# Kernel tuning notes

Measured on AMD Instinct MI355X. Metric: run time of the kernel, lower is better.

The kernel has to match this reference:

```python
import jax, jax.numpy as jnp
import numpy as np

EPS = 1e-6
K = 20  # n_knn from init


def _vnt_weight(W):
    # VNT linear: rows normalized to sum to 1 (which_norm_VNT='norm') for translation equivariance
    return W / jnp.sum(W, axis=1, keepdims=True)


def _lin(W, x):
    # apply [out,in] weight over channel axis 1 of x: [B, C_in, 3, ...] -> [B, C_out, 3, ...]
    return jnp.einsum('oi,bi...->bo...', W, x)


def _vn_lrelu(x, Wf, Wd, vnt=False):
    # VN(T)LinearLeakyReLU with negative_slope=0.0, no batchnorm. Vector axis is axis 2.
    Wp = _vnt_weight(Wf) if vnt else Wf
    p = _lin(Wp, x)
    d = _lin(Wd, x)
    dot = jnp.sum(p * d, axis=2, keepdims=True)
    dsq = jnp.sum(d * d, axis=2, keepdims=True)
    return jnp.where(dot >= 0, p, p - (dot / (dsq + EPS)) * d)


def _knn(pts, k):
    # pts: [B,N,3] -> indices of k nearest (self included), via -||xi-xj||^2 top_k
    sq = jnp.sum(pts * pts, axis=-1)                      # [B,N]
    inner = jnp.einsum('bnd,bmd->bnm', pts, pts)          # [B,N,N]
    neg_dist = 2.0 * inner - sq[:, :, None] - sq[:, None, :]
    return jax.lax.top_k(neg_dist, k)[1]                  # [B,N,k]


def _graph_feature_cross(x, k):
    # x: [B,3,N] -> edge features [B, 3(feat: nbr-ctr, ctr, cross), 3(vec), N, k]
    pts = jnp.transpose(x, (0, 2, 1))                     # [B,N,3]
    idx = _knn(pts, k)                                    # [B,N,k]
    nbr = jax.vmap(lambda p, i: p[i])(pts, idx)           # [B,N,k,3]
    ctr = jnp.broadcast_to(pts[:, :, None, :], nbr.shape)
    cross = jnp.cross(nbr, ctr)
    feat = jnp.stack([nbr - ctr, ctr, cross], axis=3)     # [B,N,k,3feat,3vec]
    return jnp.transpose(feat, (0, 3, 4, 1, 2))           # [B,3feat,3vec,N,k]


def _forward(x, Wpos_f, Wpos_d, Wc1_f, Wc1_d, Wc2_f, Wc2_d, Wt_f, Wt_d, W1_f, W1_d, W2_f, W2_d, W3):
    feat = _graph_feature_cross(x, K)                     # [B,3,3,N,K]
    h = _vn_lrelu(feat, Wpos_f, Wpos_d, vnt=True)         # [B,64,3,N,K]
    h = h.mean(axis=-1)                                   # mean pool over k -> [B,64,3,N]
    x2 = _vn_lrelu(h, Wc1_f, Wc1_d, vnt=True)             # conv_center_
    xc = _vn_lrelu(x2, Wc2_f, Wc2_d, vnt=True)            # conv_center
    tx = _vn_lrelu(xc, Wt_f, Wt_d, vnt=True)              # conv_trans [B,12,3,N]
    trans_latent = tx.mean(axis=-1)                       # [B,12,3]
    h = h - xc                                            # center features
    h = _vn_lrelu(h, W1_f, W1_d)                          # conv1
    h = _vn_lrelu(h, W2_f, W2_d)                          # conv2
    h = _lin(W3, h)                                       # conv3 (plain VNLinear) [B,116,3,N]
    rot_latent = h.mean(axis=-1)                          # [B,116,3]
    return jnp.concatenate([rot_latent, trans_latent], axis=1)  # [B,128,3]


def setup_inputs() -> dict:
    key = jax.random.key(0)
    ks = jax.random.split(key, 16)
    B, N, C = 4, 4096, 64
    ROT = 116  # c_dim - trans_c_dim

    def w(k, o, i):
        return jax.random.normal(k, (o, i), jnp.float32) * 0.1

    def wt(k, o, i):
        # VNT weights: row sums kept near 1 so normalization is well-conditioned
        return jax.random.normal(k, (o, i), jnp.float32) * 0.02 + 1.0 / i

    return {
        'x': jax.random.normal(ks[0], (B, 3, N), jnp.float32),
        'Wpos_f': wt(ks[1], C, 3), 'Wpos_d': w(ks[2], C, 3),
        'Wc1_f': wt(ks[3], C, C), 'Wc1_d': w(ks[4], C, C),
        'Wc2_f': wt(ks[5], C, C), 'Wc2_d': w(ks[6], C, C),
        'Wt_f': wt(ks[7], 12, C), 'Wt_d': w(ks[8], 12, C),
        'W1_f': w(ks[9], C, C), 'W1_d': w(ks[10], C, C),
        'W2_f': w(ks[11], C, C), 'W2_d': w(ks[12], C, C),
        'W3': w(ks[13], ROT, C),
    }


def reference(x, Wpos_f, Wpos_d, Wc1_f, Wc1_d, Wc2_f, Wc2_d, Wt_f, Wt_d, W1_f, W1_d, W2_f, W2_d, W3):
    return _forward(x, Wpos_f, Wpos_d, Wc1_f, Wc1_d, Wc2_f, Wc2_d, Wt_f, Wt_d, W1_f, W1_d, W2_f, W2_d, W3)
```

## Files before the change

### kernel.cpp

```cpp
#include <hip/hip_runtime.h>

#define NPTS 4096
#define BATCH 4
#define KNN 20
#define ROT 116

__device__ __forceinline__ void vn_lrelu3(float p[3], const float d[3]) {
  float dot = p[0]*d[0] + p[1]*d[1] + p[2]*d[2];
  if (dot < 0.0f) {
    float dsq = d[0]*d[0] + d[1]*d[1] + d[2]*d[2];
    float r = dot / (dsq + 1e-6f);
    p[0] -= r*d[0]; p[1] -= r*d[1]; p[2] -= r*d[2];
  }
}

__global__ __launch_bounds__(256) void knn_edge2_kernel(const float* __restrict__ x,
                                                        const float* __restrict__ Wf,
                                                        const float* __restrict__ Wd,
                                                        float* __restrict__ h) {
  const int blk = blockIdx.x;
  const int rowA = blk << 1, rowB = rowA + 1;
  const int b = rowA >> 12;
  const int iA = rowA & (NPTS - 1), iB = rowB & (NPTS - 1);
  const float* __restrict__ xb = x + b * 3 * NPTS;
  const float cxA = xb[iA], cyA = xb[NPTS + iA], czA = xb[2 * NPTS + iA];
  const float cxB = xb[iB], cyB = xb[NPTS + iB], czB = xb[2 * NPTS + iB];
  const int t = threadIdx.x;
  const int j0 = t << 4;

  __shared__ unsigned int hist[2048];
  __shared__ unsigned int ldA_[384], ldB_[384];
  __shared__ int ljA_[384], ljB_[384];
  __shared__ unsigned int lcount;
  __shared__ int s_BA, s_BB;
  __shared__ unsigned int wtot[4];
  __shared__ int s_nbrA[KNN], s_nbrB[KNN];
  __shared__ float eA[KNN][3][3], eB[KNN][3][3];
  __shared__ float partA[2][64][3], partB[2][64][3];

  for (int k = t; k < 2048; k += 256) hist[k] = 0u;
  if (t == 0) lcount = 0u;
  __syncthreads();

  unsigned int dbA[16], dbB[16];
#pragma unroll
  for (int q = 0; q < 4; ++q) {
    const float4 px = *(const float4*)(xb + j0 + 4 * q);
    const float4 py = *(const float4*)(xb + NPTS + j0 + 4 * q);
    const float4 pz = *(const float4*)(xb + 2 * NPTS + j0 + 4 * q);
    float dx, dy, dz, dd;
    dx = px.x - cxA; dy = py.x - cyA; dz = pz.x - czA;
    dd = dx*dx + dy*dy + dz*dz; dbA[4*q+0] = __float_as_uint(dd);
    dx = px.y - cxA; dy = py.y - cyA; dz = pz.y - czA;
    dd = dx*dx + dy*dy + dz*dz; dbA[4*q+1] = __float_as_uint(dd);
    dx = px.z - cxA; dy = py.z - cyA; dz = pz.z - czA;
    dd = dx*dx + dy*dy + dz*dz; dbA[4*q+2] = __float_as_uint(dd);
    dx = px.w - cxA; dy = py.w - cyA; dz = pz.w - czA;
    dd = dx*dx + dy*dy + dz*dz; dbA[4*q+3] = __float_as_uint(dd);
    dx = px.x - cxB; dy = py.x - cyB; dz = pz.x - czB;
    dd = dx*dx + dy*dy + dz*dz; dbB[4*q+0] = __float_as_uint(dd);
    dx = px.y - cxB; dy = py.y - cyB; dz = pz.y - czB;
    dd = dx*dx + dy*dy + dz*dz; dbB[4*q+1] = __float_as_uint(dd);
    dx = px.z - cxB; dy = py.z - cyB; dz = pz.z - czB;
    dd = dx*dx + dy*dy + dz*dz; dbB[4*q+2] = __float_as_uint(dd);
    dx = px.w - cxB; dy = py.w - cyB; dz = pz.w - czB;
    dd = dx*dx + dy*dy + dz*dz; dbB[4*q+3] = __float_as_uint(dd);
  }
#pragma unroll
  for (int s = 0; s < 16; ++s) {
    atomicAdd(&hist[dbA[s] >> 20], 1u);
    atomicAdd(&hist[dbB[s] >> 20], 0x10000u);
  }
  __syncthreads();

  unsigned int v = 0;
#pragma unroll
  for (int s = 0; s < 8; ++s) v += hist[t * 8 + s];
  const unsigned int myps = v;
  const int lane = t & 63;
#pragma unroll
  for (int off = 1; off < 64; off <<= 1) {
    unsigned int n = (unsigned int)__shfl_up((int)v, off);
    if (lane >= off) v += n;
  }
  if (lane == 63) wtot[t >> 6] = v;
  __syncthreads();
  unsigned int woff = 0;
#pragma unroll
  for (int w = 0; w < 4; ++w) if (w < (t >> 6)) woff += wtot[w];
  const unsigned int cum_in = v + woff;
  const unsigned int cum_ex = cum_in - myps;
  {
    const int ci = (int)(cum_in & 0xffffu), ce = (int)(cum_ex & 0xffffu);
    if (ce < KNN && ci >= KNN) {
      int cum = ce, B = t * 8;
      for (int s = 0; s < 8; ++s) {
        const int hh = (int)(hist[t * 8 + s] & 0xffffu);
        if (cum + hh >= KNN) { B = t * 8 + s; break; }
        cum += hh;
      }
      s_BA = B;
    }
  }
  {
    const int ci = (int)(cum_in >> 16), ce = (int)(cum_ex >> 16);
    if (ce < KNN && ci >= KNN) {
      int cum = ce, B = t * 8;
      for (int s = 0; s < 8; ++s) {
        const int hh = (int)(hist[t * 8 + s] >> 16);
        if (cum + hh >= KNN) { B = t * 8 + s; break; }
        cum += hh;
      }
      s_BB = B;
    }
  }
  __syncthreads();
  const unsigned int BA = (unsigned int)s_BA, BB = (unsigned int)s_BB;
#pragma unroll
  for (int s = 0; s < 16; ++s) {
    if ((dbA[s] >> 20) <= BA) {
      unsigned int old = atomicAdd(&lcount, 1u);
      unsigned int pos = old & 0xffffu;
      if (pos < 384u) { ldA_[pos] = dbA[s]; ljA_[pos] = j0 + s; }
    }
    if ((dbB[s] >> 20) <= BB) {
      unsigned int old = atomicAdd(&lcount, 0x10000u);
      unsigned int pos = old >> 16;
      if (pos < 384u) { ldB_[pos] = dbB[s]; ljB_[pos] = j0 + s; }
    }
  }
  __syncthreads();
  const int nA = min((int)(lcount & 0xffffu), 384);
  const int nB = min((int)(lcount >> 16), 384);
  if (t < 128) {
    for (int idx = t; idx < nA; idx += 128) {
      const unsigned int kd = ldA_[idx]; const int kj = ljA_[idx];
      int rank = 0;
      for (int m = 0; m < nA; ++m) {
        const unsigned int md = ldA_[m];
        rank += (md < kd || (md == kd && ljA_[m] < kj)) ? 1 : 0;
      }
      if (rank < KNN) s_nbrA[rank] = kj;
    }
  } else {
    for (int idx = t - 128; idx < nB; idx += 128) {
      const unsigned int kd = ldB_[idx]; const int kj = ljB_[idx];
      int rank = 0;
      for (int m = 0; m < nB; ++m) {
        const unsigned int md = ldB_[m];
        rank += (md < kd || (md == kd && ljB_[m] < kj)) ? 1 : 0;
      }
      if (rank < KNN) s_nbrB[rank] = kj;
    }
  }
  __syncthreads();

  if (t < KNN) {
    const int j = s_nbrA[t];
    const float nx = xb[j], ny = xb[NPTS + j], nz = xb[2 * NPTS + j];
    eA[t][0][0] = nx - cxA; eA[t][0][1] = ny - cyA; eA[t][0][2] = nz - czA;
    eA[t][1][0] = cxA;      eA[t][1][1] = cyA;      eA[t][1][2] = czA;
    eA[t][2][0] = ny * czA - nz * cyA;
    eA[t][2][1] = nz * cxA - nx * czA;
    eA[t][2][2] = nx * cyA - ny * cxA;
  } else if (t >= 64 && t < 64 + KNN) {
    const int k = t - 64;
    const int j = s_nbrB[k];
    const float nx = xb[j], ny = xb[NPTS + j], nz = xb[2 * NPTS + j];
    eB[k][0][0] = nx - cxB; eB[k][0][1] = ny - cyB; eB[k][0][2] = nz - czB;
    eB[k][1][0] = cxB;      eB[k][1][1] = cyB;      eB[k][1][2] = czB;
    eB[k][2][0] = ny * czB - nz * cyB;
    eB[k][2][1] = nz * cxB - nx * czB;
    eB[k][2][2] = nx * cyB - ny * cxB;
  }
  __syncthreads();

  const int c = t & 63;
  const int half = t >> 7;
  const int kg = (t >> 6) & 1;
  float f0 = Wf[c * 3 + 0], f1 = Wf[c * 3 + 1], f2 = Wf[c * 3 + 2];
  const float s = 1.0f / (f0 + f1 + f2);
  f0 *= s; f1 *= s; f2 *= s;
  const float d0 = Wd[c * 3 + 0], d1 = Wd[c * 3 + 1], d2 = Wd[c * 3 + 2];
  float a0 = 0.f, a1 = 0.f, a2 = 0.f;
  const float (*e)[3][3] = (half == 0) ? eA : eB;
#pragma unroll
  for (int kk = 0; kk < 10; ++kk) {
    const int k = kg * 10 + kk;
    float pv[3], dv[3];
#pragma unroll
    for (int vv = 0; vv < 3; ++vv) {
      pv[vv] = f0 * e[k][0][vv] + f1 * e[k][1][vv] + f2 * e[k][2][vv];
      dv[vv] = d0 * e[k][0][vv] + d1 * e[k][1][vv] + d2 * e[k][2][vv];
    }
    vn_lrelu3(pv, dv);
    a0 += pv[0]; a1 += pv[1]; a2 += pv[2];
  }
  if (half == 0) { partA[kg][c][0] = a0; partA[kg][c][1] = a1; partA[kg][c][2] = a2; }
  else           { partB[kg][c][0] = a0; partB[kg][c][1] = a1; partB[kg][c][2] = a2; }
  __syncthreads();
  if (t < 64) {
    const float inv = 1.0f / KNN;
    float* hp = h + (size_t)rowA * 192 + t * 3;
#pragma unroll
    for (int vv = 0; vv < 3; ++vv)
      hp[vv] = (partA[0][t][vv] + partA[1][t][vv]) * inv;
  } else if (t < 128) {
    const int cc = t - 64;
    const float inv = 1.0f / KNN;
    float* hp = h + (size_t)rowB * 192 + cc * 3;
#pragma unroll
    for (int vv = 0; vv < 3; ++vv)
      hp[vv] = (partB[0][cc][vv] + partB[1][cc][vv]) * inv;
  }
}

template<bool VNT, int MODE>
__global__ __launch_bounds__(256) void layer_batch(
    const float* in, float* out, float* aux,
    const float* __restrict__ Wf, const float* __restrict__ Wd) {
  __shared__ float wfT[64][65], wdT[64][65];
  __shared__ float act[4][4][64][4];
  const int t = threadIdx.x, q = t >> 6, c = t & 63;
  for (int e = t; e < 4096; e += 256) {
    wfT[e & 63][e >> 6] = Wf[e];
    wdT[e & 63][e >> 6] = Wd[e];
  }
  __syncthreads();
  if (VNT) {
    if (t < 64) {
      float s = 0.f;
      for (int i = 0; i < 64; ++i) s += wfT[i][t];
      s = 1.0f / s;
      for (int i = 0; i < 64; ++i) wfT[i][t] *= s;
    }
    __syncthreads();
  }
  const int pbase = (blockIdx.x * 4 + q) * 8;
  float r0 = 0.f, r1 = 0.f, r2 = 0.f;
  for (int pass = 0; pass < 2; ++pass) {
    const int p0 = pbase + pass * 4;
#pragma unroll
    for (int p = 0; p < 4; ++p) {
      const float* ip = in + (size_t)(p0 + p) * 192 + c * 3;
      *(float4*)act[q][p][c] = make_float4(ip[0], ip[1], ip[2], 0.f);
    }
    __builtin_amdgcn_wave_barrier();
    float af[12], ad[12];
#pragma unroll
    for (int e = 0; e < 12; ++e) { af[e] = 0.f; ad[e] = 0.f; }
    for (int i = 0; i < 64; ++i) {
      const float wfv = wfT[i][c];
      const float wdv = wdT[i][c];
#pragma unroll
      for (int p = 0; p < 4; ++p) {
        const float4 hv = *(const float4*)act[q][p][i];
        af[p*3+0] += wfv * hv.x; af[p*3+1] += wfv * hv.y; af[p*3+2] += wfv * hv.z;
        ad[p*3+0] += wdv * hv.x; ad[p*3+1] += wdv * hv.y; ad[p*3+2] += wdv * hv.z;
      }
    }
    __builtin_amdgcn_wave_barrier();
#pragma unroll
    for (int p = 0; p < 4; ++p) {
      float pf[3] = { af[p*3+0], af[p*3+1], af[p*3+2] };
      float pd[3] = { ad[p*3+0], ad[p*3+1], ad[p*3+2] };
      vn_lrelu3(pf, pd);
      const size_t ofs = (size_t)(p0 + p) * 192 + c * 3;
      if (MODE == 0) {
        out[ofs+0] = pf[0]; out[ofs+1] = pf[1]; out[ofs+2] = pf[2];
      } else if (MODE == 1) {
        const float h0 = aux[ofs+0], h1 = aux[ofs+1], h2 = aux[ofs+2];
        aux[ofs+0] = h0 - pf[0]; aux[ofs+1] = h1 - pf[1]; aux[ofs+2] = h2 - pf[2];
        out[ofs+0] = pf[0]; out[ofs+1] = pf[1]; out[ofs+2] = pf[2];
      } else {
        r0 += pf[0]; r1 += pf[1]; r2 += pf[2];
      }
    }
    __builtin_amdgcn_wave_barrier();
  }
  if (MODE == 2) {
    *(float4*)act[q][0][c] = make_float4(r0, r1, r2, 0.f);
    __syncthreads();
    if (t < 192) {
      const int cc = t / 3, vv = t - cc * 3;
      out[blockIdx.x * 192 + t] =
          act[0][0][cc][vv] + act[1][0][cc][vv] + act[2][0][cc][vv] + act[3][0][cc][vv];
    }
  }
}

__global__ __launch_bounds__(256) void trans_kernel(
    const float* __restrict__ xc,
    const float* __restrict__ Wtf, const float* __restrict__ Wtd,
    float* __restrict__ trans_part) {
  __shared__ float wtf[12][65], wtd[12][65];
  __shared__ float xpt[4][64][4];
  __shared__ float tred[4][12][3];
  const int t = threadIdx.x, q = t >> 6, l = t & 63;
  for (int e = t; e < 768; e += 256) {
    wtf[e >> 6][e & 63] = Wtf[e]; wtd[e >> 6][e & 63] = Wtd[e];
  }
  __syncthreads();
  if (t < 12) {
    float s = 0.f;
    for (int i = 0; i < 64; ++i) s += wtf[t][i];
    s = 1.0f / s;
    for (int i = 0; i < 64; ++i) wtf[t][i] *= s;
  }
  __syncthreads();
  const int cch = l >> 2, v = l & 3;
  const bool act = (cch < 12) && (v < 3);
  float ta = 0.f;
  const int pbase = (blockIdx.x * 4 + q) * 8;
  for (int g = 0; g < 8; ++g) {
    const float* xp = xc + (size_t)(pbase + g) * 192 + l * 3;
    xpt[q][l][0] = xp[0]; xpt[q][l][1] = xp[1]; xpt[q][l][2] = xp[2];
    __builtin_amdgcn_wave_barrier();
    float pf = 0.f, pd = 0.f;
    if (act) {
      for (int i = 0; i < 64; ++i) {
        const float a = xpt[q][i][v];
        pf += wtf[cch][i] * a;
        pd += wtd[cch][i] * a;
      }
    }
    float pp = pf * pd, dd = pd * pd;
    pp += __shfl_xor(pp, 1); pp += __shfl_xor(pp, 2);
    dd += __shfl_xor(dd, 1); dd += __shfl_xor(dd, 2);
    if (pp < 0.f) pf -= (pp / (dd + 1e-6f)) * pd;
    ta += pf;
    __builtin_amdgcn_wave_barrier();
  }
  if (act) { tred[q][cch][v] = ta; }
  __syncthreads();
  if (t < 36) {
    const int cc = t / 3, vv = t - cc * 3;
    trans_part[blockIdx.x * 36 + t] =
        tred[0][cc][vv] + tred[1][cc][vv] + tred[2][cc][vv] + tred[3][cc][vv];
  }
}

__global__ __launch_bounds__(384) void finalize_kernel(const float* __restrict__ rot_part,
                                                       const float* __restrict__ trans_part,
                                                       const float* __restrict__ W3,
                                                       float* __restrict__ out) {
  const int b = blockIdx.x;
  const int t = threadIdx.x;
  __shared__ float hsum[64][3];
  if (t < 192) {
    float s = 0.f;
    for (int blk = 0; blk < 128; ++blk)
      s += rot_part[(b * 128 + blk) * 192 + t];
    hsum[t / 3][t % 3] = s * (1.0f / NPTS);
  } else if (t < 228) {
    const int tt = t - 192;
    float s = 0.f;
    for (int blk = 0; blk < 128; ++blk)
      s += trans_part[(b * 128 + blk) * 36 + tt];
    out[b * 384 + 348 + tt] = s * (1.0f / NPTS);
  }
  __syncthreads();
  if (t < 348) {
    const int ch = t / 3, v = t - ch * 3;
    float s = 0.f;
    for (int i = 0; i < 64; ++i) s += W3[ch * 64 + i] * hsum[i][v];
    out[b * 384 + t] = s;
  }
}

extern "C" void kernel_launch(void* const* d_in, const int* in_sizes, int n_in,
                              void* d_out, int out_size, void* d_ws, size_t ws_size,
                              hipStream_t stream) {
  (void)in_sizes; (void)n_in; (void)out_size; (void)ws_size;
  const float* x     = (const float*)d_in[0];
  const float* Wposf = (const float*)d_in[1];
  const float* Wposd = (const float*)d_in[2];
  const float* Wc1f  = (const float*)d_in[3];
  const float* Wc1d  = (const float*)d_in[4];
  const float* Wc2f  = (const float*)d_in[5];
  const float* Wc2d  = (const float*)d_in[6];
  const float* Wtf   = (const float*)d_in[7];
  const float* Wtd   = (const float*)d_in[8];
  const float* W1f   = (const float*)d_in[9];
  const float* W1d   = (const float*)d_in[10];
  const float* W2f   = (const float*)d_in[11];
  const float* W2d   = (const float*)d_in[12];
  const float* W3    = (const float*)d_in[13];
  float* out = (float*)d_out;

  char* ws = (char*)d_ws;
  float* P          = (float*)(ws + 1310720);
  float* Q          = (float*)(ws + 13893632);
  float* trans_part = (float*)(ws + 26476544);
  float* rot_part   = (float*)(ws + 26550272);

  knn_edge2_kernel<<<BATCH * NPTS / 2, 256, 0, stream>>>(x, Wposf, Wposd, P);
  layer_batch<true, 0><<<512, 256, 0, stream>>>(P, Q, nullptr, Wc1f, Wc1d);
  layer_batch<true, 1><<<512, 256, 0, stream>>>(Q, Q, P, Wc2f, Wc2d);
  trans_kernel<<<512, 256, 0, stream>>>(Q, Wtf, Wtd, trans_part);
  layer_batch<false, 0><<<512, 256, 0, stream>>>(P, P, nullptr, W1f, W1d);
  layer_batch<false, 2><<<512, 256, 0, stream>>>(P, rot_part, nullptr, W2f, W2d);
  finalize_kernel<<<BATCH, 384, 0, stream>>>(rot_part, trans_part, W3, out);
}
```

Measured before the change: 204.7 us.

## Fuse per-point VN layer chain and trans head into one kernel

Replaces the four layer_batch launches and the trans kernel with a single chain kernel that keeps each point's intermediate features in registers and reloads only the weights into shared memory between stages. This removes the global writes and reads of the Q and P intermediates and the launch gaps between kernels. In exchange, register pressure per thread rises sharply and the stages within a block run strictly in sequence, which can lower occupancy.

```diff
diff --git a/kernel.cpp b/kernel.cpp
--- a/kernel.cpp
+++ b/kernel.cpp
@@ -215,127 +215,230 @@
   }
 }
 
-template<bool VNT, int MODE>
-__global__ __launch_bounds__(256) void layer_batch(
-    const float* in, float* out, float* aux,
-    const float* __restrict__ Wf, const float* __restrict__ Wd) {
+__global__ __launch_bounds__(256) void chain_kernel(
+    const float* __restrict__ hin,
+    const float* __restrict__ Wc1f, const float* __restrict__ Wc1d,
+    const float* __restrict__ Wc2f, const float* __restrict__ Wc2d,
+    const float* __restrict__ Wtf,  const float* __restrict__ Wtd,
+    const float* __restrict__ W1f,  const float* __restrict__ W1d,
+    const float* __restrict__ W2f,  const float* __restrict__ W2d,
+    float* __restrict__ rot_part, float* __restrict__ trans_part) {
   __shared__ float wfT[64][65], wdT[64][65];
   __shared__ float act[4][4][64][4];
+  __shared__ float tred[4][12][3];
   const int t = threadIdx.x, q = t >> 6, c = t & 63;
-  for (int e = t; e < 4096; e += 256) {
-    wfT[e & 63][e >> 6] = Wf[e];
-    wdT[e & 63][e >> 6] = Wd[e];
-  }
-  __syncthreads();
-  if (VNT) {
-    if (t < 64) {
-      float s = 0.f;
-      for (int i = 0; i < 64; ++i) s += wfT[i][t];
-      s = 1.0f / s;
-      for (int i = 0; i < 64; ++i) wfT[i][t] *= s;
-    }
-    __syncthreads();
-  }
   const int pbase = (blockIdx.x * 4 + q) * 8;
-  float r0 = 0.f, r1 = 0.f, r2 = 0.f;
+
+  float hx[8], hy[8], hz[8];
+  float x2x[8], x2y[8], x2z[8];
+  float xcx[8], xcy[8], xcz[8];
+
+  for (int e = t; e < 4096; e += 256) { wfT[e&63][e>>6] = Wc1f[e]; wdT[e&63][e>>6] = Wc1d[e]; }
+  __syncthreads();
+  if (t < 64) {
+    float s = 0.f;
+    for (int i = 0; i < 64; ++i) s += wfT[i][t];
+    s = 1.0f / s;
+    for (int i = 0; i < 64; ++i) wfT[i][t] *= s;
+  }
+  __syncthreads();
+#pragma unroll
   for (int pass = 0; pass < 2; ++pass) {
-    const int p0 = pbase + pass * 4;
-#pragma unroll
-    for (int p = 0; p < 4; ++p) {
-      const float* ip = in + (size_t)(p0 + p) * 192 + c * 3;
-      *(float4*)act[q][p][c] = make_float4(ip[0], ip[1], ip[2], 0.f);
+#pragma unroll
+    for (int p = 0; p < 4; ++p) {
+      const int pp = pass * 4 + p;
+      const float* ip = hin + (size_t)(pbase + pp) * 192 + c * 3;
+      hx[pp] = ip[0]; hy[pp] = ip[1]; hz[pp] = ip[2];
+      *(float4*)act[q][p][c] = make_float4(hx[pp], hy[pp], hz[pp], 0.f);
     }
     __builtin_amdgcn_wave_barrier();
     float af[12], ad[12];
 #pragma unroll
-    for (int e = 0; e < 12; ++e) { af[e] = 0.f; ad[e] = 0.f; }
+    for (int e2 = 0; e2 < 12; ++e2) { af[e2] = 0.f; ad[e2] = 0.f; }
     for (int i = 0; i < 64; ++i) {
-      const float wfv = wfT[i][c];
-      const float wdv = wdT[i][c];
+      const float wfv = wfT[i][c], wdv = wdT[i][c];
 #pragma unroll
       for (int p = 0; p < 4; ++p) {
         const float4 hv = *(const float4*)act[q][p][i];
-        af[p*3+0] += wfv * hv.x; af[p*3+1] += wfv * hv.y; af[p*3+2] += wfv * hv.z;
-        ad[p*3+0] += wdv * hv.x; ad[p*3+1] += wdv * hv.y; ad[p*3+2] += wdv * hv.z;
-      }
-    }
-    __builtin_amdgcn_wave_barrier();
-#pragma unroll
-    for (int p = 0; p < 4; ++p) {
-      float pf[3] = { af[p*3+0], af[p*3+1], af[p*3+2] };
-      float pd[3] = { ad[p*3+0], ad[p*3+1], ad[p*3+2] };
+        af[p*3+0] += wfv*hv.x; af[p*3+1] += wfv*hv.y; af[p*3+2] += wfv*hv.z;
+        ad[p*3+0] += wdv*hv.x; ad[p*3+1] += wdv*hv.y; ad[p*3+2] += wdv*hv.z;
+      }
+    }
+    __builtin_amdgcn_wave_barrier();
+#pragma unroll
+    for (int p = 0; p < 4; ++p) {
+      const int pp = pass * 4 + p;
+      float pf[3] = { af[p*3], af[p*3+1], af[p*3+2] };
+      float pd[3] = { ad[p*3], ad[p*3+1], ad[p*3+2] };
       vn_lrelu3(pf, pd);
-      const size_t ofs = (size_t)(p0 + p) * 192 + c * 3;
-      if (MODE == 0) {
-        out[ofs+0] = pf[0]; out[ofs+1] = pf[1]; out[ofs+2] = pf[2];
-      } else if (MODE == 1) {
-        const float h0 = aux[ofs+0], h1 = aux[ofs+1], h2 = aux[ofs+2];
-        aux[ofs+0] = h0 - pf[0]; aux[ofs+1] = h1 - pf[1]; aux[ofs+2] = h2 - pf[2];
-        out[ofs+0] = pf[0]; out[ofs+1] = pf[1]; out[ofs+2] = pf[2];
-      } else {
-        r0 += pf[0]; r1 += pf[1]; r2 += pf[2];
-      }
-    }
-    __builtin_amdgcn_wave_barrier();
-  }
-  if (MODE == 2) {
-    *(float4*)act[q][0][c] = make_float4(r0, r1, r2, 0.f);
-    __syncthreads();
-    if (t < 192) {
-      const int cc = t / 3, vv = t - cc * 3;
-      out[blockIdx.x * 192 + t] =
-          act[0][0][cc][vv] + act[1][0][cc][vv] + act[2][0][cc][vv] + act[3][0][cc][vv];
-    }
-  }
-}
-
-__global__ __launch_bounds__(256) void trans_kernel(
-    const float* __restrict__ xc,
-    const float* __restrict__ Wtf, const float* __restrict__ Wtd,
-    float* __restrict__ trans_part) {
-  __shared__ float wtf[12][65], wtd[12][65];
-  __shared__ float xpt[4][64][4];
-  __shared__ float tred[4][12][3];
-  const int t = threadIdx.x, q = t >> 6, l = t & 63;
-  for (int e = t; e < 768; e += 256) {
-    wtf[e >> 6][e & 63] = Wtf[e]; wtd[e >> 6][e & 63] = Wtd[e];
-  }
+      x2x[pp] = pf[0]; x2y[pp] = pf[1]; x2z[pp] = pf[2];
+    }
+  }
+
+  __syncthreads();
+  for (int e = t; e < 4096; e += 256) { wfT[e&63][e>>6] = Wc2f[e]; wdT[e&63][e>>6] = Wc2d[e]; }
+  __syncthreads();
+  if (t < 64) {
+    float s = 0.f;
+    for (int i = 0; i < 64; ++i) s += wfT[i][t];
+    s = 1.0f / s;
+    for (int i = 0; i < 64; ++i) wfT[i][t] *= s;
+  }
+  __syncthreads();
+#pragma unroll
+  for (int pass = 0; pass < 2; ++pass) {
+#pragma unroll
+    for (int p = 0; p < 4; ++p) {
+      const int pp = pass * 4 + p;
+      *(float4*)act[q][p][c] = make_float4(x2x[pp], x2y[pp], x2z[pp], 0.f);
+    }
+    __builtin_amdgcn_wave_barrier();
+    float af[12], ad[12];
+#pragma unroll
+    for (int e2 = 0; e2 < 12; ++e2) { af[e2] = 0.f; ad[e2] = 0.f; }
+    for (int i = 0; i < 64; ++i) {
+      const float wfv = wfT[i][c], wdv = wdT[i][c];
+#pragma unroll
+      for (int p = 0; p < 4; ++p) {
+        const float4 hv = *(const float4*)act[q][p][i];
+        af[p*3+0] += wfv*hv.x; af[p*3+1] += wfv*hv.y; af[p*3+2] += wfv*hv.z;
+        ad[p*3+0] += wdv*hv.x; ad[p*3+1] += wdv*hv.y; ad[p*3+2] += wdv*hv.z;
+      }
+    }
+    __builtin_amdgcn_wave_barrier();
+#pragma unroll
+    for (int p = 0; p < 4; ++p) {
+      const int pp = pass * 4 + p;
+      float pf[3] = { af[p*3], af[p*3+1], af[p*3+2] };
+      float pd[3] = { ad[p*3], ad[p*3+1], ad[p*3+2] };
+      vn_lrelu3(pf, pd);
+      xcx[pp] = pf[0]; xcy[pp] = pf[1]; xcz[pp] = pf[2];
+      hx[pp] -= pf[0]; hy[pp] -= pf[1]; hz[pp] -= pf[2];
+    }
+  }
+
+  __syncthreads();
+  for (int e = t; e < 768; e += 256) { wfT[e&63][e>>6] = Wtf[e]; wdT[e&63][e>>6] = Wtd[e]; }
   __syncthreads();
   if (t < 12) {
     float s = 0.f;
-    for (int i = 0; i < 64; ++i) s += wtf[t][i];
+    for (int i = 0; i < 64; ++i) s += wfT[i][t];
     s = 1.0f / s;
-    for (int i = 0; i < 64; ++i) wtf[t][i] *= s;
-  }
-  __syncthreads();
-  const int cch = l >> 2, v = l & 3;
-  const bool act = (cch < 12) && (v < 3);
-  float ta = 0.f;
-  const int pbase = (blockIdx.x * 4 + q) * 8;
-  for (int g = 0; g < 8; ++g) {
-    const float* xp = xc + (size_t)(pbase + g) * 192 + l * 3;
-    xpt[q][l][0] = xp[0]; xpt[q][l][1] = xp[1]; xpt[q][l][2] = xp[2];
-    __builtin_amdgcn_wave_barrier();
-    float pf = 0.f, pd = 0.f;
-    if (act) {
-      for (int i = 0; i < 64; ++i) {
-        const float a = xpt[q][i][v];
-        pf += wtf[cch][i] * a;
-        pd += wtd[cch][i] * a;
-      }
-    }
-    float pp = pf * pd, dd = pd * pd;
-    pp += __shfl_xor(pp, 1); pp += __shfl_xor(pp, 2);
-    dd += __shfl_xor(dd, 1); dd += __shfl_xor(dd, 2);
-    if (pp < 0.f) pf -= (pp / (dd + 1e-6f)) * pd;
-    ta += pf;
-    __builtin_amdgcn_wave_barrier();
-  }
-  if (act) { tred[q][cch][v] = ta; }
-  __syncthreads();
-  if (t < 36) {
+    for (int i = 0; i < 64; ++i) wfT[i][t] *= s;
+  }
+  __syncthreads();
+  {
+    const int cch = c >> 2, vv = c & 3;
+    const bool actv = (cch < 12) && (vv < 3);
+    float ta = 0.f;
+#pragma unroll
+    for (int pass = 0; pass < 2; ++pass) {
+#pragma unroll
+      for (int p = 0; p < 4; ++p) {
+        const int pp = pass * 4 + p;
+        *(float4*)act[q][p][c] = make_float4(xcx[pp], xcy[pp], xcz[pp], 0.f);
+      }
+      __builtin_amdgcn_wave_barrier();
+#pragma unroll
+      for (int p = 0; p < 4; ++p) {
+        float pf = 0.f, pd = 0.f;
+        if (actv) {
+          for (int i = 0; i < 64; ++i) {
+            const float a = act[q][p][i][vv];
+            pf += wfT[i][cch] * a;
+            pd += wdT[i][cch] * a;
+          }
+        }
+        float pp2 = pf * pd, dd = pd * pd;
+        pp2 += __shfl_xor(pp2, 1); pp2 += __shfl_xor(pp2, 2);
+        dd  += __shfl_xor(dd, 1);  dd  += __shfl_xor(dd, 2);
+        if (pp2 < 0.f) pf -= (pp2 / (dd + 1e-6f)) * pd;
+        ta += pf;
+      }
+      __builtin_amdgcn_wave_barrier();
+    }
+    if (actv) { tred[q][cch][vv] = ta; }
+  }
+
+  __syncthreads();
+  for (int e = t; e < 4096; e += 256) { wfT[e&63][e>>6] = W1f[e]; wdT[e&63][e>>6] = W1d[e]; }
+  __syncthreads();
+#pragma unroll
+  for (int pass = 0; pass < 2; ++pass) {
+#pragma unroll
+    for (int p = 0; p < 4; ++p) {
+      const int pp = pass * 4 + p;
+      *(float4*)act[q][p][c] = make_float4(hx[pp], hy[pp], hz[pp], 0.f);
+    }
+    __builtin_amdgcn_wave_barrier();
+    float af[12], ad[12];
+#pragma unroll
+    for (int e2 = 0; e2 < 12; ++e2) { af[e2] = 0.f; ad[e2] = 0.f; }
+    for (int i = 0; i < 64; ++i) {
+      const float wfv = wfT[i][c], wdv = wdT[i][c];
+#pragma unroll
+      for (int p = 0; p < 4; ++p) {
+        const float4 hv = *(const float4*)act[q][p][i];
+        af[p*3+0] += wfv*hv.x; af[p*3+1] += wfv*hv.y; af[p*3+2] += wfv*hv.z;
+        ad[p*3+0] += wdv*hv.x; ad[p*3+1] += wdv*hv.y; ad[p*3+2] += wdv*hv.z;
+      }
+    }
+    __builtin_amdgcn_wave_barrier();
+#pragma unroll
+    for (int p = 0; p < 4; ++p) {
+      const int pp = pass * 4 + p;
+      float pf[3] = { af[p*3], af[p*3+1], af[p*3+2] };
+      float pd[3] = { ad[p*3], ad[p*3+1], ad[p*3+2] };
+      vn_lrelu3(pf, pd);
+      x2x[pp] = pf[0]; x2y[pp] = pf[1]; x2z[pp] = pf[2];
+    }
+  }
+
+  __syncthreads();
+  for (int e = t; e < 4096; e += 256) { wfT[e&63][e>>6] = W2f[e]; wdT[e&63][e>>6] = W2d[e]; }
+  __syncthreads();
+  float r0 = 0.f, r1 = 0.f, r2 = 0.f;
+#pragma unroll
+  for (int pass = 0; pass < 2; ++pass) {
+#pragma unroll
+    for (int p = 0; p < 4; ++p) {
+      const int pp = pass * 4 + p;
+      *(float4*)act[q][p][c] = make_float4(x2x[pp], x2y[pp], x2z[pp], 0.f);
+    }
+    __builtin_amdgcn_wave_barrier();
+    float af[12], ad[12];
+#pragma unroll
+    for (int e2 = 0; e2 < 12; ++e2) { af[e2] = 0.f; ad[e2] = 0.f; }
+    for (int i = 0; i < 64; ++i) {
+      const float wfv = wfT[i][c], wdv = wdT[i][c];
+#pragma unroll
+      for (int p = 0; p < 4; ++p) {
+        const float4 hv = *(const float4*)act[q][p][i];
+        af[p*3+0] += wfv*hv.x; af[p*3+1] += wfv*hv.y; af[p*3+2] += wfv*hv.z;
+        ad[p*3+0] += wdv*hv.x; ad[p*3+1] += wdv*hv.y; ad[p*3+2] += wdv*hv.z;
+      }
+    }
+    __builtin_amdgcn_wave_barrier();
+#pragma unroll
+    for (int p = 0; p < 4; ++p) {
+      float pf[3] = { af[p*3], af[p*3+1], af[p*3+2] };
+      float pd[3] = { ad[p*3], ad[p*3+1], ad[p*3+2] };
+      vn_lrelu3(pf, pd);
+      r0 += pf[0]; r1 += pf[1]; r2 += pf[2];
+    }
+    __builtin_amdgcn_wave_barrier();
+  }
+
+  *(float4*)act[q][0][c] = make_float4(r0, r1, r2, 0.f);
+  __syncthreads();
+  if (t < 192) {
     const int cc = t / 3, vv = t - cc * 3;
-    trans_part[blockIdx.x * 36 + t] =
+    rot_part[blockIdx.x * 192 + t] =
+        act[0][0][cc][vv] + act[1][0][cc][vv] + act[2][0][cc][vv] + act[3][0][cc][vv];
+  } else if (t >= 192 && t < 228) {
+    const int tt = t - 192;
+    const int cc = tt / 3, vv = tt - cc * 3;
+    trans_part[blockIdx.x * 36 + tt] =
         tred[0][cc][vv] + tred[1][cc][vv] + tred[2][cc][vv] + tred[3][cc][vv];
   }
 }
@@ -390,15 +493,11 @@
 
   char* ws = (char*)d_ws;
   float* P          = (float*)(ws + 1310720);
-  float* Q          = (float*)(ws + 13893632);
   float* trans_part = (float*)(ws + 26476544);
   float* rot_part   = (float*)(ws + 26550272);
 
   knn_edge2_kernel<<<BATCH * NPTS / 2, 256, 0, stream>>>(x, Wposf, Wposd, P);
-  layer_batch<true, 0><<<512, 256, 0, stream>>>(P, Q, nullptr, Wc1f, Wc1d);
-  layer_batch<true, 1><<<512, 256, 0, stream>>>(Q, Q, P, Wc2f, Wc2d);
-  trans_kernel<<<512, 256, 0, stream>>>(Q, Wtf, Wtd, trans_part);
-  layer_batch<false, 0><<<512, 256, 0, stream>>>(P, P, nullptr, W1f, W1d);
-  layer_batch<false, 2><<<512, 256, 0, stream>>>(P, rot_part, nullptr, W2f, W2d);
+  chain_kernel<<<512, 256, 0, stream>>>(P, Wc1f, Wc1d, Wc2f, Wc2d, Wtf, Wtd,
+                                        W1f, W1d, W2f, W2d, rot_part, trans_part);
   finalize_kernel<<<BATCH, 384, 0, stream>>>(rot_part, trans_part, W3, out);
 }
```

New measurement: 183.4 us, median of 2. 1.12x faster.
